# Optimization experiments

Measured on AMD Instinct MI355X. Metric: run time of the kernel, lower is better.

The kernel has to match this reference:

```python
import jax, jax.numpy as jnp
import numpy as np

B, X_DIM, Y_DIM, HIDDEN = 512, 768, 128, 1024
H2 = HIDDEN // 2


def setup_inputs() -> dict:
    key = jax.random.key(0)
    ks = jax.random.split(key, 10)
    s_in = 1.0 / np.sqrt(X_DIM)
    s_h = 1.0 / np.sqrt(H2)
    return {
        "x_samples": jax.random.normal(ks[0], (B, X_DIM), jnp.float32),
        "y_samples": jax.random.normal(ks[1], (B, Y_DIM), jnp.float32),
        "w1_mu": jax.random.uniform(ks[2], (X_DIM, H2), jnp.float32, -s_in, s_in),
        "b1_mu": jax.random.uniform(ks[3], (H2,), jnp.float32, -s_in, s_in),
        "w2_mu": jax.random.uniform(ks[4], (H2, Y_DIM), jnp.float32, -s_h, s_h),
        "b2_mu": jax.random.uniform(ks[5], (Y_DIM,), jnp.float32, -s_h, s_h),
        "w1_lv": jax.random.uniform(ks[6], (X_DIM, H2), jnp.float32, -s_in, s_in),
        "b1_lv": jax.random.uniform(ks[7], (H2,), jnp.float32, -s_in, s_in),
        "w2_lv": jax.random.uniform(ks[8], (H2, Y_DIM), jnp.float32, -s_h, s_h),
        "b2_lv": jax.random.uniform(ks[9], (Y_DIM,), jnp.float32, -s_h, s_h),
    }


def reference(x_samples, y_samples, w1_mu, b1_mu, w2_mu, b2_mu,
              w1_lv, b1_lv, w2_lv, b2_lv):
    batch = y_samples.shape[0]
    # p_mu / p_logvar MLP heads
    mu = jax.nn.relu(x_samples @ w1_mu + b1_mu) @ w2_mu + b2_mu          # [B, Y]
    logvar = jnp.tanh(jax.nn.relu(x_samples @ w1_lv + b1_lv) @ w2_lv + b2_lv)  # [B, Y]

    inv_var = jnp.exp(-logvar)
    # positive: diagonal Gaussian log-prob of y_i under p(.|x_i), up to const
    positive = (-0.5 * (mu - y_samples) ** 2 * inv_var - 0.5 * logvar).sum(-1)  # [B]

    # pairwise log-probs: row i = params from x_i, col j = sample y_j
    mu_1 = mu[:, None, :]            # [B, 1, Y]
    lv_1 = logvar[:, None, :]        # [B, 1, Y]
    y_1 = y_samples[None, :, :]      # [1, B, Y]
    all_probs = (-0.5 * (y_1 - mu_1) ** 2 * jnp.exp(-lv_1) - 0.5 * lv_1).sum(-1)  # [B, B]

    # Faithful replication of the torch broadcasting: diag_mask is [B, B, 1],
    # so all_probs + diag_mask broadcasts to [B, B, B], then logsumexp over dim 0.
    diag_mask = (jnp.eye(batch, dtype=all_probs.dtype) * -20.0)[:, :, None]  # [B, B, 1]
    logits = all_probs + diag_mask                                           # [B, B, B]
    negative = jax.scipy.special.logsumexp(logits, axis=0) - jnp.log(batch - 1.0)  # [B, B]

    return (positive - negative).mean()
```

## Files before the change

kernel.cpp:

```cpp
#include <hip/hip_runtime.h>
#include <math.h>

#define BSZ   512
#define XD    768
#define YD    128
#define H2D   512

__global__ __launch_bounds__(256, 2) void layer1_kernel(
    const float* __restrict__ x,
    const float* __restrict__ w1_mu, const float* __restrict__ w1_lv,
    float* __restrict__ p1)
{
    __shared__ float As[16][132];
    __shared__ float Bs[16][132];

    const int t      = threadIdx.x;
    const int branch = blockIdx.z >> 4;
    const int ks     = blockIdx.z & 15;
    const float* __restrict__ W = branch ? w1_lv : w1_mu;
    float* __restrict__ out = p1 + (size_t)blockIdx.z * (BSZ * H2D);

    const int m0 = blockIdx.x * 128;
    const int n0 = blockIdx.y * 128;
    const int tx = t & 15;
    const int ty = t >> 4;

    const int am  = t >> 1;
    const int akq = (t & 1) * 8;
    const int bkk = t >> 4;
    const int bnq = (t & 15) * 8;

    const int kbase = ks * 48;
    float acc[8][8] = {};

    float4 a0p = *(const float4*)&x[(m0 + am) * XD + kbase + akq];
    float4 a1p = *(const float4*)&x[(m0 + am) * XD + kbase + akq + 4];
    float4 b0p = *(const float4*)&W[(kbase + bkk) * H2D + n0 + bnq];
    float4 b1p = *(const float4*)&W[(kbase + bkk) * H2D + n0 + bnq + 4];

    for (int kt = 0; kt < 48; kt += 16) {
        __syncthreads();
        As[akq + 0][am] = a0p.x; As[akq + 1][am] = a0p.y;
        As[akq + 2][am] = a0p.z; As[akq + 3][am] = a0p.w;
        As[akq + 4][am] = a1p.x; As[akq + 5][am] = a1p.y;
        As[akq + 6][am] = a1p.z; As[akq + 7][am] = a1p.w;
        *(float4*)&Bs[bkk][bnq]     = b0p;
        *(float4*)&Bs[bkk][bnq + 4] = b1p;
        __syncthreads();
        if (kt + 16 < 48) {
            const int kn = kbase + kt + 16;
            a0p = *(const float4*)&x[(m0 + am) * XD + kn + akq];
            a1p = *(const float4*)&x[(m0 + am) * XD + kn + akq + 4];
            b0p = *(const float4*)&W[(kn + bkk) * H2D + n0 + bnq];
            b1p = *(const float4*)&W[(kn + bkk) * H2D + n0 + bnq + 4];
        }
        #pragma unroll
        for (int k = 0; k < 16; ++k) {
            const float4 a0 = *(const float4*)&As[k][ty * 8];
            const float4 a1 = *(const float4*)&As[k][ty * 8 + 4];
            const float4 b0 = *(const float4*)&Bs[k][tx * 8];
            const float4 b1 = *(const float4*)&Bs[k][tx * 8 + 4];
            const float av[8] = {a0.x, a0.y, a0.z, a0.w, a1.x, a1.y, a1.z, a1.w};
            const float bv[8] = {b0.x, b0.y, b0.z, b0.w, b1.x, b1.y, b1.z, b1.w};
            #pragma unroll
            for (int i = 0; i < 8; ++i)
                #pragma unroll
                for (int j = 0; j < 8; ++j)
                    acc[i][j] += av[i] * bv[j];
        }
    }

    #pragma unroll
    for (int i = 0; i < 8; ++i) {
        const int row = (m0 + ty * 8 + i) * H2D + n0 + tx * 8;
        *(float4*)&out[row]     = make_float4(acc[i][0], acc[i][1], acc[i][2], acc[i][3]);
        *(float4*)&out[row + 4] = make_float4(acc[i][4], acc[i][5], acc[i][6], acc[i][7]);
    }
}

__global__ __launch_bounds__(256, 2) void layer2_kernel(
    const float* __restrict__ p1,
    const float* __restrict__ b1_mu, const float* __restrict__ b1_lv,
    const float* __restrict__ w2_mu, const float* __restrict__ w2_lv,
    const float* __restrict__ y,
    float* __restrict__ p2,
    double* __restrict__ Sy, double* __restrict__ Sy2,
    double* __restrict__ accum, unsigned int* __restrict__ counter)
{
    __shared__ float Hc[32][36];
    const int t = threadIdx.x;

    if (blockIdx.z == 32) {
        const int id = blockIdx.x;
        const int dl = t & 7;
        const int g  = t >> 3;
        const int d  = id * 8 + dl;
        float s = 0.f, s2 = 0.f;
        #pragma unroll
        for (int i = g * 16; i < g * 16 + 16; ++i) {
            const float v = y[i * YD + d];
            s += v; s2 += v * v;
        }
        float* shs  = &Hc[0][0];
        float* shs2 = &Hc[0][0] + 512;
        shs[t] = s; shs2[t] = s2;
        __syncthreads();
        if (t < 8) {
            double S = 0.0, S2 = 0.0;
            #pragma unroll
            for (int gg = 0; gg < 32; ++gg) {
                S += (double)shs[gg * 8 + t]; S2 += (double)shs2[gg * 8 + t];
            }
            Sy[id * 8 + t] = S; Sy2[id * 8 + t] = S2;
        } else if (id == 0 && t == 8)  { accum[0] = 0.0; }
        else if (id == 0 && t == 9)  { accum[1] = 0.0; }
        else if (id == 0 && t == 10) { *counter = 0u; }
        return;
    }

    const int branch = blockIdx.z >> 4;
    const int ks2    = blockIdx.z & 15;
    const float* __restrict__ q  = p1 + (size_t)(branch * 16) * (BSZ * H2D);
    const float* __restrict__ b1 = branch ? b1_lv : b1_mu;
    const float* __restrict__ W  = branch ? w2_lv : w2_mu;
    float* __restrict__ out = p2 + (size_t)blockIdx.z * (BSZ * YD);

    const int m0   = blockIdx.x * 32;
    const int kb   = ks2 * 32;
    const int lane = t & 63;
    const int wave = t >> 6;

    float br0[32], br1[32];
    #pragma unroll
    for (int k = 0; k < 32; ++k) {
        br0[k] = W[(kb + k) * YD + lane];
        br1[k] = W[(kb + k) * YD + 64 + lane];
    }

    {
        const int row = t >> 3;
        const int kq  = (t & 7) * 4;
        const int base = (m0 + row) * H2D + kb + kq;
        float4 h = *(const float4*)&b1[kb + kq];
        #pragma unroll
        for (int s = 0; s < 16; ++s) {
            const float4 v = *(const float4*)&q[(size_t)s * (BSZ * H2D) + base];
            h.x += v.x; h.y += v.y; h.z += v.z; h.w += v.w;
        }
        h.x = fmaxf(h.x, 0.f); h.y = fmaxf(h.y, 0.f);
        h.z = fmaxf(h.z, 0.f); h.w = fmaxf(h.w, 0.f);
        *(float4*)&Hc[row][kq] = h;
    }
    __syncthreads();

    const int wm0 = wave * 8;
    float acc0[8] = {}, acc1[8] = {};
    #pragma unroll
    for (int m = 0; m < 8; ++m) {
        const float* hrow = &Hc[wm0 + m][0];
        #pragma unroll
        for (int qd = 0; qd < 8; ++qd) {
            const float4 a4 = *(const float4*)&hrow[qd * 4];
            acc0[m] += a4.x * br0[qd * 4 + 0]; acc1[m] += a4.x * br1[qd * 4 + 0];
            acc0[m] += a4.y * br0[qd * 4 + 1]; acc1[m] += a4.y * br1[qd * 4 + 1];
            acc0[m] += a4.z * br0[qd * 4 + 2]; acc1[m] += a4.z * br1[qd * 4 + 2];
            acc0[m] += a4.w * br0[qd * 4 + 3]; acc1[m] += a4.w * br1[qd * 4 + 3];
        }
    }

    #pragma unroll
    for (int m = 0; m < 8; ++m) {
        const int row = (m0 + wm0 + m) * YD;
        out[row + lane]      = acc0[m];
        out[row + 64 + lane] = acc1[m];
    }
}

__global__ __launch_bounds__(256) void reduce_kernel(
    const float* __restrict__ p2, const float* __restrict__ y,
    const float* __restrict__ b2_mu, const float* __restrict__ b2_lv,
    const double* __restrict__ Sy, const double* __restrict__ Sy2,
    double* __restrict__ accum, unsigned int* __restrict__ counter,
    float* __restrict__ outp)
{
    const int NE = BSZ * YD;
    const int e  = blockIdx.x * 256 + threadIdx.x;
    const int d  = e & (YD - 1);

    float mu = b2_mu[d];
    float lp = b2_lv[d];
    #pragma unroll
    for (int s = 0; s < 16; ++s) {
        mu += p2[s * NE + e];
        lp += p2[(16 + s) * NE + e];
    }
    const float lv = tanhf(lp);
    const float iv = expf(-lv);
    const float dm = mu - y[e];

    double pos = -0.5 * (double)dm * (double)dm * (double)iv - 0.5 * (double)lv;
    double ap  = (double)iv * (-0.5 * Sy2[d] + (double)mu * Sy[d]
                               - 256.0 * (double)mu * (double)mu)
               - 256.0 * (double)lv;

    #pragma unroll
    for (int off = 32; off > 0; off >>= 1) {
        pos += __shfl_down(pos, off);
        ap  += __shfl_down(ap, off);
    }
    __shared__ double sp[4];
    __shared__ double sa[4];
    const int lane = threadIdx.x & 63;
    const int wv   = threadIdx.x >> 6;
    if (lane == 0) { sp[wv] = pos; sa[wv] = ap; }
    __syncthreads();
    if (threadIdx.x == 0) {
        atomicAdd(&accum[0], sp[0] + sp[1] + sp[2] + sp[3]);
        atomicAdd(&accum[1], sa[0] + sa[1] + sa[2] + sa[3]);
        __threadfence();
        const unsigned int old = atomicAdd(counter, 1u);
        if (old == 255u) {
            const double P = atomicAdd(&accum[0], 0.0);
            const double A = atomicAdd(&accum[1], 0.0);
            const double C = log1p(exp(-20.0) / 511.0);
            outp[0] = (float)(P / 512.0 - A / 262144.0 - C);
        }
    }
}

extern "C" void kernel_launch(void* const* d_in, const int* in_sizes, int n_in,
                              void* d_out, int out_size, void* d_ws, size_t ws_size,
                              hipStream_t stream) {
    const float* x     = (const float*)d_in[0];
    const float* y     = (const float*)d_in[1];
    const float* w1_mu = (const float*)d_in[2];
    const float* b1_mu = (const float*)d_in[3];
    const float* w2_mu = (const float*)d_in[4];
    const float* b2_mu = (const float*)d_in[5];
    const float* w1_lv = (const float*)d_in[6];
    const float* b1_lv = (const float*)d_in[7];
    const float* w2_lv = (const float*)d_in[8];
    const float* b2_lv = (const float*)d_in[9];

    char* ws = (char*)d_ws;
    float*  p1 = (float*)(ws);
    float*  p2 = (float*)(ws + (size_t)32 * BSZ * H2D * 4);
    double* Sy = (double*)(ws + (size_t)32 * BSZ * H2D * 4
                              + (size_t)32 * BSZ * YD * 4);
    double* Sy2 = Sy + YD;
    double* accum = Sy2 + YD;
    unsigned int* counter = (unsigned int*)(accum + 2);

    layer1_kernel<<<dim3(4, 4, 32), 256, 0, stream>>>(x, w1_mu, w1_lv, p1);
    layer2_kernel<<<dim3(16, 1, 33), 256, 0, stream>>>(
        p1, b1_mu, b1_lv, w2_mu, w2_lv, y, p2, Sy, Sy2, accum, counter);
    reduce_kernel<<<256, 256, 0, stream>>>(
        p2, y, b2_mu, b2_lv, Sy, Sy2, accum, counter, (float*)d_out);
}
```

Before: 121.6 us.

## Use smaller layer-1 tiles with fewer K splits to cut partial-sum traffic

```diff
diff --git a/kernel.cpp b/kernel.cpp
--- a/kernel.cpp
+++ b/kernel.cpp
@@ -5,76 +5,64 @@
 #define XD    768
 #define YD    128
 #define H2D   512
+
 
 __global__ __launch_bounds__(256, 2) void layer1_kernel(
     const float* __restrict__ x,
     const float* __restrict__ w1_mu, const float* __restrict__ w1_lv,
     float* __restrict__ p1)
 {
-    __shared__ float As[16][132];
-    __shared__ float Bs[16][132];
+    __shared__ float As[16][68];
+    __shared__ float Bs[16][68];
 
     const int t      = threadIdx.x;
-    const int branch = blockIdx.z >> 4;
-    const int ks     = blockIdx.z & 15;
+    const int branch = blockIdx.z >> 2;
+    const int ks     = blockIdx.z & 3;
     const float* __restrict__ W = branch ? w1_lv : w1_mu;
     float* __restrict__ out = p1 + (size_t)blockIdx.z * (BSZ * H2D);
 
-    const int m0 = blockIdx.x * 128;
-    const int n0 = blockIdx.y * 128;
+    const int m0 = blockIdx.x * 64;
+    const int n0 = blockIdx.y * 64;
     const int tx = t & 15;
     const int ty = t >> 4;
 
-    const int am  = t >> 1;
-    const int akq = (t & 1) * 8;
+    const int am  = t >> 2;
+    const int akq = (t & 3) * 4;
     const int bkk = t >> 4;
-    const int bnq = (t & 15) * 8;
-
-    const int kbase = ks * 48;
-    float acc[8][8] = {};
-
-    float4 a0p = *(const float4*)&x[(m0 + am) * XD + kbase + akq];
-    float4 a1p = *(const float4*)&x[(m0 + am) * XD + kbase + akq + 4];
-    float4 b0p = *(const float4*)&W[(kbase + bkk) * H2D + n0 + bnq];
-    float4 b1p = *(const float4*)&W[(kbase + bkk) * H2D + n0 + bnq + 4];
-
-    for (int kt = 0; kt < 48; kt += 16) {
+    const int bnq = (t & 15) * 4;
+
+    const int kbase = ks * 192;
+    float acc[4][4] = {};
+
+    float4 ap = *(const float4*)&x[(m0 + am) * XD + kbase + akq];
+    float4 bp = *(const float4*)&W[(kbase + bkk) * H2D + n0 + bnq];
+
+    for (int kt = 0; kt < 192; kt += 16) {
         __syncthreads();
-        As[akq + 0][am] = a0p.x; As[akq + 1][am] = a0p.y;
-        As[akq + 2][am] = a0p.z; As[akq + 3][am] = a0p.w;
-        As[akq + 4][am] = a1p.x; As[akq + 5][am] = a1p.y;
-        As[akq + 6][am] = a1p.z; As[akq + 7][am] = a1p.w;
-        *(float4*)&Bs[bkk][bnq]     = b0p;
-        *(float4*)&Bs[bkk][bnq + 4] = b1p;
+        As[akq + 0][am] = ap.x; As[akq + 1][am] = ap.y;
+        As[akq + 2][am] = ap.z; As[akq + 3][am] = ap.w;
+        *(float4*)&Bs[bkk][bnq] = bp;
         __syncthreads();
-        if (kt + 16 < 48) {
+        if (kt + 16 < 192) {
             const int kn = kbase + kt + 16;
-            a0p = *(const float4*)&x[(m0 + am) * XD + kn + akq];
-            a1p = *(const float4*)&x[(m0 + am) * XD + kn + akq + 4];
-            b0p = *(const float4*)&W[(kn + bkk) * H2D + n0 + bnq];
-            b1p = *(const float4*)&W[(kn + bkk) * H2D + n0 + bnq + 4];
+            ap = *(const float4*)&x[(m0 + am) * XD + kn + akq];
+            bp = *(const float4*)&W[(kn + bkk) * H2D + n0 + bnq];
         }
         #pragma unroll
         for (int k = 0; k < 16; ++k) {
-            const float4 a0 = *(const float4*)&As[k][ty * 8];
-            const float4 a1 = *(const float4*)&As[k][ty * 8 + 4];
-            const float4 b0 = *(const float4*)&Bs[k][tx * 8];
-            const float4 b1 = *(const float4*)&Bs[k][tx * 8 + 4];
-            const float av[8] = {a0.x, a0.y, a0.z, a0.w, a1.x, a1.y, a1.z, a1.w};
-            const float bv[8] = {b0.x, b0.y, b0.z, b0.w, b1.x, b1.y, b1.z, b1.w};
-            #pragma unroll
-            for (int i = 0; i < 8; ++i)
-                #pragma unroll
-                for (int j = 0; j < 8; ++j)
-                    acc[i][j] += av[i] * bv[j];
-        }
-    }
-
-    #pragma unroll
-    for (int i = 0; i < 8; ++i) {
-        const int row = (m0 + ty * 8 + i) * H2D + n0 + tx * 8;
-        *(float4*)&out[row]     = make_float4(acc[i][0], acc[i][1], acc[i][2], acc[i][3]);
-        *(float4*)&out[row + 4] = make_float4(acc[i][4], acc[i][5], acc[i][6], acc[i][7]);
+            const float4 a4 = *(const float4*)&As[k][ty * 4];
+            const float4 b4 = *(const float4*)&Bs[k][tx * 4];
+            acc[0][0] += a4.x*b4.x; acc[0][1] += a4.x*b4.y; acc[0][2] += a4.x*b4.z; acc[0][3] += a4.x*b4.w;
+            acc[1][0] += a4.y*b4.x; acc[1][1] += a4.y*b4.y; acc[1][2] += a4.y*b4.z; acc[1][3] += a4.y*b4.w;
+            acc[2][0] += a4.z*b4.x; acc[2][1] += a4.z*b4.y; acc[2][2] += a4.z*b4.z; acc[2][3] += a4.z*b4.w;
+            acc[3][0] += a4.w*b4.x; acc[3][1] += a4.w*b4.y; acc[3][2] += a4.w*b4.z; acc[3][3] += a4.w*b4.w;
+        }
+    }
+
+    #pragma unroll
+    for (int i = 0; i < 4; ++i) {
+        const float4 o = make_float4(acc[i][0], acc[i][1], acc[i][2], acc[i][3]);
+        *(float4*)&out[(m0 + ty * 4 + i) * H2D + n0 + tx * 4] = o;
     }
 }
 
@@ -87,10 +75,10 @@
     double* __restrict__ Sy, double* __restrict__ Sy2,
     double* __restrict__ accum, unsigned int* __restrict__ counter)
 {
-    __shared__ float Hc[32][36];
+    __shared__ float Hc[32][68];
     const int t = threadIdx.x;
 
-    if (blockIdx.z == 32) {
+    if (blockIdx.z == 16) {
         const int id = blockIdx.x;
         const int dl = t & 7;
         const int g  = t >> 3;
@@ -118,53 +106,62 @@
         return;
     }
 
-    const int branch = blockIdx.z >> 4;
-    const int ks2    = blockIdx.z & 15;
-    const float* __restrict__ q  = p1 + (size_t)(branch * 16) * (BSZ * H2D);
+    const int branch = blockIdx.z >> 3;
+    const int ks     = blockIdx.z & 7;
+    const float* __restrict__ q  = p1 + (size_t)(branch * 4) * (BSZ * H2D);
     const float* __restrict__ b1 = branch ? b1_lv : b1_mu;
     const float* __restrict__ W  = branch ? w2_lv : w2_mu;
     float* __restrict__ out = p2 + (size_t)blockIdx.z * (BSZ * YD);
 
     const int m0   = blockIdx.x * 32;
-    const int kb   = ks2 * 32;
+    const int kb   = ks * 64;
     const int lane = t & 63;
     const int wave = t >> 6;
 
-    float br0[32], br1[32];
-    #pragma unroll
-    for (int k = 0; k < 32; ++k) {
-        br0[k] = W[(kb + k) * YD + lane];
-        br1[k] = W[(kb + k) * YD + 64 + lane];
-    }
-
     {
-        const int row = t >> 3;
-        const int kq  = (t & 7) * 4;
+        const int row  = t >> 3;
+        const int kq   = (t & 7) * 8;
         const int base = (m0 + row) * H2D + kb + kq;
-        float4 h = *(const float4*)&b1[kb + kq];
-        #pragma unroll
-        for (int s = 0; s < 16; ++s) {
-            const float4 v = *(const float4*)&q[(size_t)s * (BSZ * H2D) + base];
-            h.x += v.x; h.y += v.y; h.z += v.z; h.w += v.w;
-        }
-        h.x = fmaxf(h.x, 0.f); h.y = fmaxf(h.y, 0.f);
-        h.z = fmaxf(h.z, 0.f); h.w = fmaxf(h.w, 0.f);
-        *(float4*)&Hc[row][kq] = h;
+        float4 h0 = *(const float4*)&b1[kb + kq];
+        float4 h1 = *(const float4*)&b1[kb + kq + 4];
+        #pragma unroll
+        for (int s = 0; s < 4; ++s) {
+            const float4 v0 = *(const float4*)&q[(size_t)s * (BSZ * H2D) + base];
+            const float4 v1 = *(const float4*)&q[(size_t)s * (BSZ * H2D) + base + 4];
+            h0.x += v0.x; h0.y += v0.y; h0.z += v0.z; h0.w += v0.w;
+            h1.x += v1.x; h1.y += v1.y; h1.z += v1.z; h1.w += v1.w;
+        }
+        h0.x = fmaxf(h0.x, 0.f); h0.y = fmaxf(h0.y, 0.f);
+        h0.z = fmaxf(h0.z, 0.f); h0.w = fmaxf(h0.w, 0.f);
+        h1.x = fmaxf(h1.x, 0.f); h1.y = fmaxf(h1.y, 0.f);
+        h1.z = fmaxf(h1.z, 0.f); h1.w = fmaxf(h1.w, 0.f);
+        *(float4*)&Hc[row][kq]     = h0;
+        *(float4*)&Hc[row][kq + 4] = h1;
     }
     __syncthreads();
 
     const int wm0 = wave * 8;
     float acc0[8] = {}, acc1[8] = {};
     #pragma unroll
-    for (int m = 0; m < 8; ++m) {
-        const float* hrow = &Hc[wm0 + m][0];
-        #pragma unroll
-        for (int qd = 0; qd < 8; ++qd) {
-            const float4 a4 = *(const float4*)&hrow[qd * 4];
-            acc0[m] += a4.x * br0[qd * 4 + 0]; acc1[m] += a4.x * br1[qd * 4 + 0];
-            acc0[m] += a4.y * br0[qd * 4 + 1]; acc1[m] += a4.y * br1[qd * 4 + 1];
-            acc0[m] += a4.z * br0[qd * 4 + 2]; acc1[m] += a4.z * br1[qd * 4 + 2];
-            acc0[m] += a4.w * br0[qd * 4 + 3]; acc1[m] += a4.w * br1[qd * 4 + 3];
+    for (int half = 0; half < 2; ++half) {
+        const int kh = kb + half * 32;
+        float br0[32], br1[32];
+        #pragma unroll
+        for (int k = 0; k < 32; ++k) {
+            br0[k] = W[(kh + k) * YD + lane];
+            br1[k] = W[(kh + k) * YD + 64 + lane];
+        }
+        #pragma unroll
+        for (int m = 0; m < 8; ++m) {
+            const float* hrow = &Hc[wm0 + m][half * 32];
+            #pragma unroll
+            for (int qd = 0; qd < 8; ++qd) {
+                const float4 a4 = *(const float4*)&hrow[qd * 4];
+                acc0[m] += a4.x * br0[qd * 4 + 0]; acc1[m] += a4.x * br1[qd * 4 + 0];
+                acc0[m] += a4.y * br0[qd * 4 + 1]; acc1[m] += a4.y * br1[qd * 4 + 1];
+                acc0[m] += a4.z * br0[qd * 4 + 2]; acc1[m] += a4.z * br1[qd * 4 + 2];
+                acc0[m] += a4.w * br0[qd * 4 + 3]; acc1[m] += a4.w * br1[qd * 4 + 3];
+            }
         }
     }
 
@@ -190,9 +187,9 @@
     float mu = b2_mu[d];
     float lp = b2_lv[d];
     #pragma unroll
-    for (int s = 0; s < 16; ++s) {
+    for (int s = 0; s < 8; ++s) {
         mu += p2[s * NE + e];
-        lp += p2[(16 + s) * NE + e];
+        lp += p2[(8 + s) * NE + e];
     }
     const float lv = tanhf(lp);
     const float iv = expf(-lv);
@@ -244,15 +241,15 @@
 
     char* ws = (char*)d_ws;
     float*  p1 = (float*)(ws);
-    float*  p2 = (float*)(ws + (size_t)32 * BSZ * H2D * 4);
-    double* Sy = (double*)(ws + (size_t)32 * BSZ * H2D * 4
-                              + (size_t)32 * BSZ * YD * 4);
+    float*  p2 = (float*)(ws + (size_t)8 * BSZ * H2D * 4);
+    double* Sy = (double*)(ws + (size_t)8 * BSZ * H2D * 4
+                              + (size_t)16 * BSZ * YD * 4);
     double* Sy2 = Sy + YD;
     double* accum = Sy2 + YD;
     unsigned int* counter = (unsigned int*)(accum + 2);
 
-    layer1_kernel<<<dim3(4, 4, 32), 256, 0, stream>>>(x, w1_mu, w1_lv, p1);
-    layer2_kernel<<<dim3(16, 1, 33), 256, 0, stream>>>(
+    layer1_kernel<<<dim3(8, 8, 8), 256, 0, stream>>>(x, w1_mu, w1_lv, p1);
+    layer2_kernel<<<dim3(16, 1, 17), 256, 0, stream>>>(
         p1, b1_mu, b1_lv, w2_mu, w2_lv, y, p2, Sy, Sy2, accum, counter);
     reduce_kernel<<<256, 256, 0, stream>>>(
         p2, y, b2_mu, b2_lv, Sy, Sy2, accum, counter, (float*)d_out);
```

Result: faster. 111.5 us (-8.3%).
